# Kernel tuning notes

Hardware: AMD Instinct MI355X
Metric: run time of the kernel (lower is better)

Reference implementation:

```python
import jax, jax.numpy as jnp
import numpy as np
from jax import lax

T, D, HID, C = 16384, 1024, 1024, 16
H = HID // 2  # per-direction hidden size


def _uniform(key, shape, bound):
    return jax.random.uniform(key, shape, jnp.float32, -bound, bound)


def setup_inputs() -> dict:
    key = jax.random.key(0)
    ks = jax.random.split(key, 16)
    s = 1.0 / np.sqrt(H)        # PyTorch LSTM init bound
    sl = 1.0 / np.sqrt(HID)     # PyTorch Linear init bound
    return {
        "sequence": jax.random.normal(ks[0], (T, D), jnp.float32),
        "h0": jax.random.normal(ks[1], (2, 1, H), jnp.float32),
        "c0": jax.random.normal(ks[2], (2, 1, H), jnp.float32),
        "w_ih_f": _uniform(ks[3], (4 * H, D), s),
        "w_hh_f": _uniform(ks[4], (4 * H, H), s),
        "b_ih_f": _uniform(ks[5], (4 * H,), s),
        "b_hh_f": _uniform(ks[6], (4 * H,), s),
        "w_ih_b": _uniform(ks[7], (4 * H, D), s),
        "w_hh_b": _uniform(ks[8], (4 * H, H), s),
        "b_ih_b": _uniform(ks[9], (4 * H,), s),
        "b_hh_b": _uniform(ks[10], (4 * H,), s),
        "w_lin": _uniform(ks[11], (C, HID), sl),
        "b_lin": _uniform(ks[12], (C,), sl),
        "transitions": jax.random.uniform(ks[13], (C, C), jnp.float32),  # torch.rand
    }


def _lstm_scan(x, h0, c0, w_ih, w_hh, b_ih, b_hh, reverse):
    # x: [T, D]; PyTorch gate order: i, f, g, o
    def step(carry, xt):
        h, c = carry
        g = w_ih @ xt + b_ih + w_hh @ h + b_hh  # [4H]
        i, f, gg, o = jnp.split(g, 4)
        i = jax.nn.sigmoid(i)
        f = jax.nn.sigmoid(f)
        gg = jnp.tanh(gg)
        o = jax.nn.sigmoid(o)
        c = f * c + i * gg
        h = o * jnp.tanh(c)
        return (h, c), h
    _, hs = lax.scan(step, (h0, c0), x, reverse=reverse)
    return hs  # [T, H], hs[t] = hidden at time t (aligned for both directions)


def _viterbi(feats, transitions):
    # feats: [T, C]; init forward_var = zeros (per the original torch.full(..., 0))
    def vstep(fv, feat):
        scores = fv[None, :] + transitions          # [C_next, C_prev]
        bp = jnp.argmax(scores, axis=1)             # backpointers
        fv2 = jnp.max(scores, axis=1) + feat
        return fv2, bp
    fv, bps = lax.scan(vstep, jnp.zeros((C,), feats.dtype), feats)
    best = jnp.argmax(fv)
    path_score = fv[best]
    def bstep(b, bp_row):
        nb = bp_row[b]
        return nb, nb
    _, rev = lax.scan(bstep, best, bps, reverse=True)  # rev[t] = state before step t's transition
    best_path = jnp.concatenate([rev, best[None]])     # length T+1, matches torch output
    return path_score, best_path


def reference(sequence, h0, c0, w_ih_f, w_hh_f, b_ih_f, b_hh_f,
              w_ih_b, w_hh_b, b_ih_b, b_hh_b, w_lin, b_lin, transitions):
    hs_f = _lstm_scan(sequence, h0[0, 0], c0[0, 0], w_ih_f, w_hh_f, b_ih_f, b_hh_f, False)
    hs_b = _lstm_scan(sequence, h0[1, 0], c0[1, 0], w_ih_b, w_hh_b, b_ih_b, b_hh_b, True)
    lstm_out = jnp.concatenate([hs_f, hs_b], axis=-1)   # [T, HID]
    feats = lstm_out @ w_lin.T + b_lin                  # [T, C]
    return _viterbi(feats, transitions)
```

## Files before the change

kernel.cpp:

```cpp
#include <hip/hip_runtime.h>

#define T_STEPS 16384
#define CSTEPS  1024
#define NCHUNK  16
#define DMODEL  1024
#define HID     512
#define G4      2048
#define NC      16
#define NGEMMB  192

#define POLL_GUARD (1 << 18)

static const size_t OFF_Z     = 0;
static const size_t OFF_HF    = 8388608ull;
static const size_t OFF_HB    = 16777216ull;
static const size_t OFF_FEATS = 25165824ull;
static const size_t FLOATS_TOTAL = 25427968ull;
static const size_t OFF_BP_B  = FLOATS_TOTAL * 4ull;
static const size_t OFF_P_B   = OFF_BP_B + 262144ull;
static const size_t OFF_EX_B  = OFF_P_B + 262144ull;
static const size_t OFF_CTR_B = OFF_EX_B + 16384ull;
static const size_t NEED_B    = OFF_CTR_B + 1024ull;

__device__ __forceinline__ float sigm_fast(float x) { return 1.0f / (1.0f + __expf(-x)); }
__device__ __forceinline__ float tanh_fast(float x) { return 1.0f - 2.0f / (__expf(2.0f * x) + 1.0f); }

__global__ __launch_bounds__(256, 1) void fused_kernel(
    const float* __restrict__ seq,
    const float* __restrict__ wih_f, const float* __restrict__ bih_f, const float* __restrict__ bhh_f,
    const float* __restrict__ wih_b, const float* __restrict__ bih_b, const float* __restrict__ bhh_b,
    const float* __restrict__ whh_f, const float* __restrict__ whh_b,
    const float* __restrict__ h0, const float* __restrict__ c0,
    float* __restrict__ hf, float* __restrict__ hb,
    float* __restrict__ Zbuf,
    unsigned long long* __restrict__ exf,
    unsigned int* __restrict__ gemm_done, unsigned int* __restrict__ recur_prog)
{
    const int bid = blockIdx.x;
    const int tid = threadIdx.x;
    const int pk  = bid & 7;

    if (pk < 2) {
        const int dir = pk;
        const int g   = bid >> 3;
        const float* whh = dir ? whh_b : whh_f;
        float* hout      = dir ? hb : hf;
        unsigned long long* ex = dir ? (exf + 1024) : exf;

        const int w = tid >> 6, lane = tid & 63;
        const int G = lane >> 4, u = lane & 15;
        const int R = 512 * G + 16 * g + u;

        float wreg[128];
        {
            const float* src = &whh[(size_t)R * HID + w * 128];
            #pragma unroll
            for (int j = 0; j < 32; ++j) {
                float4 v = *(const float4*)&src[j * 4];
                wreg[j*4+0]=v.x; wreg[j*4+1]=v.y; wreg[j*4+2]=v.z; wreg[j*4+3]=v.w;
            }
        }

        __shared__ __align__(16) float h_lds[512];
        __shared__ __align__(16) float p_lds[2][256];

        float cst = 0.f;
        if (w == 0 && lane < 16) cst = c0[dir * HID + 16 * g + lane];

        {
            const int i0 = 128 * w + 2 * lane;
            h_lds[i0]     = h0[dir * HID + i0];
            h_lds[i0 + 1] = h0[dir * HID + i0 + 1];
        }

        int dead = 0;
        const float* Zd = Zbuf + (size_t)dir * 2 * CSTEPS * G4;
        float zr_cur = 0.f, zr_pref = 0.f;

        for (int s = 0; s < T_STEPS; ++s) {
            const int par = s & 1;
            if ((s & (CSTEPS - 1)) == 0) {
                if (tid == 0) {
                    const int cg = s >> 10;
                    int guard = 0; unsigned int gd;
                    do {
                        gd = __hip_atomic_load(&gemm_done[cg], __ATOMIC_RELAXED,
                                               __HIP_MEMORY_SCOPE_AGENT);
                        if (++guard > (1 << 20)) { dead = 1; break; }
                    } while (gd < (unsigned)NGEMMB);
                }
                if (__syncthreads_or(dead)) break;
                if (w == 1) {
                    const int rr = dir ? (1023 - (s & 1023)) : (s & 1023);
                    zr_cur = __hip_atomic_load(
                        &Zd[((size_t)((s >> 10) & 1) * CSTEPS + rr) * G4 + R],
                        __ATOMIC_RELAXED, __HIP_MEMORY_SCOPE_AGENT);
                }
            } else if (w == 1) {
                zr_cur = zr_pref;
            }

            if (s > 0) {
                const int i0   = 128 * w + 2 * lane;
                const int base = par * 512 + i0;
                const unsigned long long want = (unsigned long long)(unsigned)s;
                unsigned long long v0, v1;
                int guard = 0;
                for (;;) {
                    v0 = __hip_atomic_load(&ex[base],     __ATOMIC_RELAXED, __HIP_MEMORY_SCOPE_AGENT);
                    v1 = __hip_atomic_load(&ex[base + 1], __ATOMIC_RELAXED, __HIP_MEMORY_SCOPE_AGENT);
                    if (((v0 >> 32) == want) & ((v1 >> 32) == want)) break;
                    if (++guard > POLL_GUARD) { dead = 1; break; }
                }
                union { unsigned int ui; float f; } ca, cb;
                ca.ui = (unsigned int)v0; cb.ui = (unsigned int)v1;
                h_lds[i0]     = ca.f;
                h_lds[i0 + 1] = cb.f;
            }

            float a0 = 0.f, a1 = 0.f, a2 = 0.f, a3 = 0.f;
            {
                const float4* h4 = (const float4*)&h_lds[w * 128];
                #pragma unroll
                for (int j = 0; j < 8; ++j) {
                    float4 h_0 = h4[4*j+0], h_1 = h4[4*j+1], h_2 = h4[4*j+2], h_3 = h4[4*j+3];
                    a0 += wreg[16*j+ 0]*h_0.x + wreg[16*j+ 1]*h_0.y + wreg[16*j+ 2]*h_0.z + wreg[16*j+ 3]*h_0.w;
                    a1 += wreg[16*j+ 4]*h_1.x + wreg[16*j+ 5]*h_1.y + wreg[16*j+ 6]*h_1.z + wreg[16*j+ 7]*h_1.w;
                    a2 += wreg[16*j+ 8]*h_2.x + wreg[16*j+ 9]*h_2.y + wreg[16*j+10]*h_2.z + wreg[16*j+11]*h_2.w;
                    a3 += wreg[16*j+12]*h_3.x + wreg[16*j+13]*h_3.y + wreg[16*j+14]*h_3.z + wreg[16*j+15]*h_3.w;
                }
            }
            float acc = (a0 + a1) + (a2 + a3);
            if (w == 1) acc += zr_cur;
            p_lds[par][tid] = acc;
            if (w == 1 && ((s + 1) & (CSTEPS - 1)) != 0) {
                const int sn = s + 1;
                const int rr = dir ? (1023 - (sn & 1023)) : (sn & 1023);
                zr_pref = __hip_atomic_load(
                    &Zd[((size_t)((sn >> 10) & 1) * CSTEPS + rr) * G4 + R],
                    __ATOMIC_RELAXED, __HIP_MEMORY_SCOPE_AGENT);
            }
            if (__syncthreads_or(dead)) break;

            if (w == 0) {
                float rv = p_lds[par][lane] + p_lds[par][64+lane]
                         + p_lds[par][128+lane] + p_lds[par][192+lane];
                float a = (G == 2) ? tanh_fast(rv) : sigm_fast(rv);
                float ig = __shfl(a, u,      64);
                float fg = __shfl(a, u + 16, 64);
                float gg = __shfl(a, u + 32, 64);
                float og = __shfl(a, u + 48, 64);
                if (lane < 16) {
                    float cn = fg * cst + ig * gg;
                    cst = cn;
                    float hn = og * tanh_fast(cn);
                    union { float f; unsigned int ui; } cv; cv.f = hn;
                    unsigned long long pv =
                        ((unsigned long long)(unsigned)(s + 1) << 32) | (unsigned long long)cv.ui;
                    __hip_atomic_store(&ex[((s + 1) & 1) * 512 + 16 * g + lane], pv,
                                       __ATOMIC_RELAXED, __HIP_MEMORY_SCOPE_AGENT);
                    const int t = dir ? (T_STEPS - 1 - s) : s;
                    hout[(size_t)t * HID + 16 * g + lane] = hn;
                }
                if ((s & (CSTEPS - 1)) == (CSTEPS - 1) && lane == 0)
                    __hip_atomic_fetch_add(&recur_prog[s >> 10], 1u, __ATOMIC_RELAXED,
                                           __HIP_MEMORY_SCOPE_AGENT);
            }
        }
    } else {
        const int gb = (pk - 2) * 32 + (bid >> 3);
        __shared__ __align__(16) float As[16][68];
        __shared__ __align__(16) float Bs[16][68];
        const int lr = tid >> 2, ls = tid & 3, tx = tid & 15, ty = tid >> 4;

        for (int cc = 0; cc < NCHUNK; ++cc) {
            if (cc >= 2 && tid == 0) {
                int guard = 0; unsigned int rp;
                for (;;) {
                    rp = __hip_atomic_load(&recur_prog[cc - 2], __ATOMIC_RELAXED,
                                           __HIP_MEMORY_SCOPE_AGENT);
                    if (rp >= 64u) break;
                    __builtin_amdgcn_s_sleep(16);
                    if (++guard > (1 << 20)) break;
                }
            }
            __syncthreads();

            for (int tix = gb; tix < 2 * 16 * 32; tix += NGEMMB) {
                const int dr  = tix >> 9;
                const int rem = tix & 511;
                const int mt  = rem >> 5;
                const int nt  = rem & 31;
                const int t0  = dr ? (T_STEPS - (cc + 1) * CSTEPS) : (cc * CSTEPS);
                const float* W  = dr ? wih_b : wih_f;
                const float* bi = dr ? bih_b : bih_f;
                const float* bh = dr ? bhh_b : bhh_f;
                float* Zt = Zbuf + (size_t)(dr * 2 + (cc & 1)) * CSTEPS * G4;

                float acc[4][4] = {};
                for (int k0 = 0; k0 < DMODEL; k0 += 16) {
                    float4 av = *(const float4*)&seq[(size_t)(t0 + mt*64 + lr) * DMODEL + k0 + ls*4];
                    float4 bv = *(const float4*)&W[(size_t)(nt*64 + lr) * DMODEL + k0 + ls*4];
                    __syncthreads();
                    As[ls*4+0][lr]=av.x; As[ls*4+1][lr]=av.y; As[ls*4+2][lr]=av.z; As[ls*4+3][lr]=av.w;
                    Bs[ls*4+0][lr]=bv.x; Bs[ls*4+1][lr]=bv.y; Bs[ls*4+2][lr]=bv.z; Bs[ls*4+3][lr]=bv.w;
                    __syncthreads();
                    #pragma unroll
                    for (int k = 0; k < 16; ++k) {
                        float4 a = *(const float4*)&As[k][ty * 4];
                        float4 b = *(const float4*)&Bs[k][tx * 4];
                        acc[0][0]+=a.x*b.x; acc[0][1]+=a.x*b.y; acc[0][2]+=a.x*b.z; acc[0][3]+=a.x*b.w;
                        acc[1][0]+=a.y*b.x; acc[1][1]+=a.y*b.y; acc[1][2]+=a.y*b.z; acc[1][3]+=a.y*b.w;
                        acc[2][0]+=a.z*b.x; acc[2][1]+=a.z*b.y; acc[2][2]+=a.z*b.z; acc[2][3]+=a.z*b.w;
                        acc[3][0]+=a.w*b.x; acc[3][1]+=a.w*b.y; acc[3][2]+=a.w*b.z; acc[3][3]+=a.w*b.w;
                    }
                }
                float4 b4  = *(const float4*)&bi[nt * 64 + tx * 4];
                float4 c4v = *(const float4*)&bh[nt * 64 + tx * 4];
                float bx=b4.x+c4v.x, by=b4.y+c4v.y, bz=b4.z+c4v.z, bw_=b4.w+c4v.w;
                #pragma unroll
                for (int i = 0; i < 4; ++i) {
                    float4 o;
                    o.x=acc[i][0]+bx; o.y=acc[i][1]+by; o.z=acc[i][2]+bz; o.w=acc[i][3]+bw_;
                    *(float4*)&Zt[(size_t)(mt*64 + ty*4 + i) * G4 + nt*64 + tx*4] = o;
                }
            }
            __threadfence();
            __syncthreads();
            if (tid == 0)
                __hip_atomic_fetch_add(&gemm_done[cc], 1u, __ATOMIC_RELEASE,
                                       __HIP_MEMORY_SCOPE_AGENT);
        }
    }
}

__global__ __launch_bounds__(256) void feats_kernel(
    const float* __restrict__ hf, const float* __restrict__ hb,
    const float* __restrict__ wlin, const float* __restrict__ blin,
    float* __restrict__ feats)
{
    const int t = blockIdx.x;
    __shared__ __align__(16) float hl[1024];
    const int tid = threadIdx.x;
    {
        const float* src = (tid < 128) ? &hf[(size_t)t * HID + tid * 4]
                                       : &hb[(size_t)t * HID + (tid - 128) * 4];
        *(float4*)&hl[tid * 4] = *(const float4*)src;
    }
    __syncthreads();
    const int c = tid >> 4, p = tid & 15;
    float s = 0.0f;
    #pragma unroll
    for (int j = 0; j < 16; ++j) {
        float4 h4 = *(const float4*)&hl[p * 4 + j * 64];
        float4 w4 = *(const float4*)&wlin[(size_t)c * 1024 + p * 4 + j * 64];
        s += h4.x*w4.x + h4.y*w4.y + h4.z*w4.z + h4.w*w4.w;
    }
    s += __shfl_down(s, 8, 16);
    s += __shfl_down(s, 4, 16);
    s += __shfl_down(s, 2, 16);
    s += __shfl_down(s, 1, 16);
    if (p == 0) feats[t * NC + c] = s + blin[c];
}

__global__ __launch_bounds__(64) void viterbi_kernel(
    const float* __restrict__ feats, const float* __restrict__ trans,
    unsigned char* __restrict__ bp, float* __restrict__ out,
    unsigned int* __restrict__ bT)
{
    __shared__ __align__(16) float fl[4096];
    __shared__ __align__(16) float fvs[16];
    const int l = threadIdx.x;
    float tr[16];
    if (l < 16) {
        #pragma unroll
        for (int j = 0; j < 16; ++j) tr[j] = trans[l * 16 + j];
    }
    float fv = 0.0f;
    for (int cb = 0; cb < 64; ++cb) {
        #pragma unroll
        for (int j = 0; j < 16; ++j)
            *(float4*)&fl[j * 256 + l * 4] =
                *(const float4*)&feats[cb * 4096 + j * 256 + l * 4];
        __syncthreads();
        if (l < 16) {
            for (int k = 0; k < 256; ++k) {
                float m = __shfl(fv, 0, 16) + tr[0];
                int bi = 0;
                #pragma unroll
                for (int j = 1; j < 16; ++j) {
                    float sc = __shfl(fv, j, 16) + tr[j];
                    if (sc > m) { m = sc; bi = j; }
                }
                bp[(size_t)(cb * 256 + k) * 16 + l] = (unsigned char)bi;
                fv = m + fl[k * 16 + l];
            }
        }
        __syncthreads();
    }
    if (l < 16) fvs[l] = fv;
    __syncthreads();
    if (l == 0) {
        float best = fvs[0]; int bi = 0;
        #pragma unroll
        for (int j = 1; j < 16; ++j) if (fvs[j] > best) { best = fvs[j]; bi = j; }
        out[0] = best;
        out[1 + T_STEPS] = (float)bi;
        *bT = (unsigned int)bi;
    }
}

__global__ __launch_bounds__(64) void maps_kernel(
    const unsigned char* __restrict__ bp, unsigned char* __restrict__ P)
{
    const int j = blockIdx.x;
    const int l = threadIdx.x;
    __shared__ __align__(16) unsigned char lb[4096];
    __shared__ __align__(16) unsigned char lp[4096];
    #pragma unroll
    for (int i = 0; i < 4; ++i)
        *(uint4*)&lb[i * 1024 + l * 16] = *(const uint4*)&bp[(size_t)j * 4096 + i * 1024 + l * 16];
    __syncthreads();
    if (l < 16) {
        int cur = l;
        for (int k = 255; k >= 0; --k) {
            cur = lb[k * 16 + cur];
            lp[k * 16 + l] = (unsigned char)cur;
        }
    }
    __syncthreads();
    #pragma unroll
    for (int i = 0; i < 4; ++i)
        *(uint4*)&P[(size_t)j * 4096 + i * 1024 + l * 16] = *(const uint4*)&lp[i * 1024 + l * 16];
}

__global__ __launch_bounds__(64) void path_kernel(
    const unsigned char* __restrict__ P, const unsigned int* __restrict__ bT,
    float* __restrict__ out)
{
    const int j = blockIdx.x;
    const int l = threadIdx.x;
    int e = (int)(*bT);
    for (int i = 63; i > j; --i) e = P[(size_t)i * 4096 + e];
    for (int k = l; k < 256; k += 64)
        out[1 + j * 256 + k] = (float)P[(size_t)j * 4096 + k * 16 + e];
}

__global__ void fb_kernel(float* out, int n, float v0) {
    int i = blockIdx.x * 256 + threadIdx.x;
    if (i < n) out[i] = (i == 0) ? v0 : 0.0f;
}

extern "C" void kernel_launch(void* const* d_in, const int* in_sizes, int n_in,
                              void* d_out, int out_size, void* d_ws, size_t ws_size,
                              hipStream_t stream) {
    const float* seq   = (const float*)d_in[0];
    const float* h0    = (const float*)d_in[1];
    const float* c0    = (const float*)d_in[2];
    const float* wih_f = (const float*)d_in[3];
    const float* whh_f = (const float*)d_in[4];
    const float* bih_f = (const float*)d_in[5];
    const float* bhh_f = (const float*)d_in[6];
    const float* wih_b = (const float*)d_in[7];
    const float* whh_b = (const float*)d_in[8];
    const float* bih_b = (const float*)d_in[9];
    const float* bhh_b = (const float*)d_in[10];
    const float* wlin  = (const float*)d_in[11];
    const float* blin  = (const float*)d_in[12];
    const float* trans = (const float*)d_in[13];
    float* out = (float*)d_out;

    if (ws_size < NEED_B) {
        fb_kernel<<<(out_size + 255) / 256, 256, 0, stream>>>(out, out_size, -(float)ws_size);
        return;
    }

    float* wsf = (float*)d_ws;
    float* Zbuf  = wsf + OFF_Z;
    float* hf    = wsf + OFF_HF;
    float* hb    = wsf + OFF_HB;
    float* feats = wsf + OFF_FEATS;
    unsigned char* bp = (unsigned char*)d_ws + OFF_BP_B;
    unsigned char* P  = (unsigned char*)d_ws + OFF_P_B;
    unsigned long long* exf = (unsigned long long*)((char*)d_ws + OFF_EX_B);
    unsigned int* ctr = (unsigned int*)((char*)d_ws + OFF_CTR_B);
    unsigned int* gemm_done  = ctr;
    unsigned int* recur_prog = ctr + 16;
    unsigned int* bT         = ctr + 32;

    hipMemsetAsync((void*)exf, 0, 16384 + 1024, stream);

    {
        void* args[] = { (void*)&seq,
                         (void*)&wih_f, (void*)&bih_f, (void*)&bhh_f,
                         (void*)&wih_b, (void*)&bih_b, (void*)&bhh_b,
                         (void*)&whh_f, (void*)&whh_b,
                         (void*)&h0, (void*)&c0,
                         (void*)&hf, (void*)&hb, (void*)&Zbuf,
                         (void*)&exf,
                         (void*)&gemm_done, (void*)&recur_prog };
        hipError_t e = hipLaunchCooperativeKernel(
            reinterpret_cast<void*>(fused_kernel), dim3(256), dim3(256),
            args, 0, stream);
        if (e != hipSuccess) {
            fused_kernel<<<256, 256, 0, stream>>>(
                seq, wih_f, bih_f, bhh_f, wih_b, bih_b, bhh_b,
                whh_f, whh_b, h0, c0, hf, hb, Zbuf, exf,
                gemm_done, recur_prog);
        }
    }

    feats_kernel<<<16384, 256, 0, stream>>>(hf, hb, wlin, blin, feats);
    viterbi_kernel<<<1, 64, 0, stream>>>(feats, trans, bp, out, bT);
    maps_kernel<<<64, 64, 0, stream>>>(bp, P);
    path_kernel<<<64, 64, 0, stream>>>(P, bT, out);
}
```

Before: 47.19 ms.

## Replace per-step block barrier with LDS flag handoff and shrink GEMM block count

The recurrent LSTM blocks drop the per-step __syncthreads: waves 1-3 write their partial sums to LDS and publish a step counter in a volatile shared array, and wave 0 spins on those flags before the gate math, keeping its own partial in a register. The chunk-ready wait on gemm_done moves into wave 1 with a short sleep, and a shared dead flag spreads timeouts across waves. The GEMM producer block count drops from 192 to 128 (blocks with pk>=6 now idle) and poll guards are tightened. The intent is to cut barrier latency on the serial critical path. The risks are LDS memory-ordering hazards in the hand-rolled handoff, spurious timeouts from the shorter guards, and slower input-projection GEMMs from fewer producer blocks.

```diff
diff --git a/kernel.cpp b/kernel.cpp
--- a/kernel.cpp
+++ b/kernel.cpp
@@ -7,9 +7,9 @@
 #define HID     512
 #define G4      2048
 #define NC      16
-#define NGEMMB  192
-
-#define POLL_GUARD (1 << 18)
+#define NGEMMB  128
+
+#define POLL_GUARD (1 << 16)
 
 static const size_t OFF_Z     = 0;
 static const size_t OFF_HF    = 8388608ull;
@@ -63,6 +63,15 @@
 
         __shared__ __align__(16) float h_lds[512];
         __shared__ __align__(16) float p_lds[2][256];
+        __shared__ int cntl[8];
+        __shared__ int deadf;
+
+        if (tid < 8) cntl[tid] = -1;
+        if (tid == 8) deadf = 0;
+        __syncthreads();
+
+        volatile int* vcnt  = (volatile int*)cntl;
+        volatile int* vdead = (volatile int*)&deadf;
 
         float cst = 0.f;
         if (w == 0 && lane < 16) cst = c0[dir * HID + 16 * g + lane];
@@ -79,25 +88,25 @@
 
         for (int s = 0; s < T_STEPS; ++s) {
             const int par = s & 1;
-            if ((s & (CSTEPS - 1)) == 0) {
-                if (tid == 0) {
+
+            if (w == 1) {
+                if ((s & (CSTEPS - 1)) == 0) {
                     const int cg = s >> 10;
                     int guard = 0; unsigned int gd;
-                    do {
+                    for (;;) {
                         gd = __hip_atomic_load(&gemm_done[cg], __ATOMIC_RELAXED,
                                                __HIP_MEMORY_SCOPE_AGENT);
-                        if (++guard > (1 << 20)) { dead = 1; break; }
-                    } while (gd < (unsigned)NGEMMB);
-                }
-                if (__syncthreads_or(dead)) break;
-                if (w == 1) {
+                        if (gd >= (unsigned)NGEMMB) break;
+                        __builtin_amdgcn_s_sleep(2);
+                        if (++guard > (1 << 16)) { dead = 1; break; }
+                    }
                     const int rr = dir ? (1023 - (s & 1023)) : (s & 1023);
                     zr_cur = __hip_atomic_load(
                         &Zd[((size_t)((s >> 10) & 1) * CSTEPS + rr) * G4 + R],
                         __ATOMIC_RELAXED, __HIP_MEMORY_SCOPE_AGENT);
-                }
-            } else if (w == 1) {
-                zr_cur = zr_pref;
+                } else {
+                    zr_cur = zr_pref;
+                }
             }
 
             if (s > 0) {
@@ -110,13 +119,17 @@
                     v0 = __hip_atomic_load(&ex[base],     __ATOMIC_RELAXED, __HIP_MEMORY_SCOPE_AGENT);
                     v1 = __hip_atomic_load(&ex[base + 1], __ATOMIC_RELAXED, __HIP_MEMORY_SCOPE_AGENT);
                     if (((v0 >> 32) == want) & ((v1 >> 32) == want)) break;
-                    if (++guard > POLL_GUARD) { dead = 1; break; }
+                    if ((++guard & 63) == 0) {
+                        if (*vdead) { dead = 1; break; }
+                        if (guard > POLL_GUARD) { *vdead = 1; dead = 1; break; }
+                    }
                 }
                 union { unsigned int ui; float f; } ca, cb;
                 ca.ui = (unsigned int)v0; cb.ui = (unsigned int)v1;
                 h_lds[i0]     = ca.f;
                 h_lds[i0 + 1] = cb.f;
             }
+            if (dead) { *vdead = 1; break; }
 
             float a0 = 0.f, a1 = 0.f, a2 = 0.f, a3 = 0.f;
             {
@@ -131,20 +144,36 @@
                 }
             }
             float acc = (a0 + a1) + (a2 + a3);
-            if (w == 1) acc += zr_cur;
-            p_lds[par][tid] = acc;
-            if (w == 1 && ((s + 1) & (CSTEPS - 1)) != 0) {
-                const int sn = s + 1;
-                const int rr = dir ? (1023 - (sn & 1023)) : (sn & 1023);
-                zr_pref = __hip_atomic_load(
-                    &Zd[((size_t)((sn >> 10) & 1) * CSTEPS + rr) * G4 + R],
-                    __ATOMIC_RELAXED, __HIP_MEMORY_SCOPE_AGENT);
-            }
-            if (__syncthreads_or(dead)) break;
-
-            if (w == 0) {
-                float rv = p_lds[par][lane] + p_lds[par][64+lane]
-                         + p_lds[par][128+lane] + p_lds[par][192+lane];
+
+            if (w != 0) {
+                if (w == 1) {
+                    acc += zr_cur;
+                    if (((s + 1) & (CSTEPS - 1)) != 0) {
+                        const int sn = s + 1;
+                        const int rr = dir ? (1023 - (sn & 1023)) : (sn & 1023);
+                        zr_pref = __hip_atomic_load(
+                            &Zd[((size_t)((sn >> 10) & 1) * CSTEPS + rr) * G4 + R],
+                            __ATOMIC_RELAXED, __HIP_MEMORY_SCOPE_AGENT);
+                    }
+                }
+                p_lds[par][64 * w + lane] = acc;
+                asm volatile("s_waitcnt lgkmcnt(0)" ::: "memory");
+                if (lane == 0) vcnt[par * 4 + w] = s;
+            } else {
+                int guard = 0;
+                for (;;) {
+                    int c1 = vcnt[par * 4 + 1];
+                    int c2 = vcnt[par * 4 + 2];
+                    int c3 = vcnt[par * 4 + 3];
+                    if ((c1 == s) & (c2 == s) & (c3 == s)) break;
+                    if ((++guard & 63) == 0) {
+                        if (*vdead) { dead = 1; break; }
+                        if (guard > (1 << 16)) { *vdead = 1; dead = 1; break; }
+                    }
+                }
+                if (dead) break;
+                float rv = acc + p_lds[par][64 + lane]
+                         + p_lds[par][128 + lane] + p_lds[par][192 + lane];
                 float a = (G == 2) ? tanh_fast(rv) : sigm_fast(rv);
                 float ig = __shfl(a, u,      64);
                 float fg = __shfl(a, u + 16, 64);
@@ -167,7 +196,8 @@
                                            __HIP_MEMORY_SCOPE_AGENT);
             }
         }
-    } else {
+        if (dead) *vdead = 1;
+    } else if (pk < 6) {
         const int gb = (pk - 2) * 32 + (bid >> 3);
         __shared__ __align__(16) float As[16][68];
         __shared__ __align__(16) float Bs[16][68];
@@ -181,7 +211,7 @@
                                            __HIP_MEMORY_SCOPE_AGENT);
                     if (rp >= 64u) break;
                     __builtin_amdgcn_s_sleep(16);
-                    if (++guard > (1 << 20)) break;
+                    if (++guard > (1 << 14)) break;
                 }
             }
             __syncthreads();
```

Result: no change. 47.72 ms (+1.1%).
